# Kernel optimization log

Measured on AMD Instinct MI355X. Metric: run time of the kernel, lower is better.

## Reference

```python
import jax, jax.numpy as jnp
import numpy as np

N = 200000   # active voxels
G = 128      # dense grid extent per axis
C = 128      # hidden channels
IN_C = 1
TEMB = 6
K = 27       # 3x3x3 kernel offsets


def _build_neighbors():
    # Sample N unique voxel coordinates in a G^3 grid and build the 27-offset
    # rulebook: neighbor_idx[k, i] = index of voxel at coord[i] + offset[k],
    # or N (sentinel -> zero-padded feature row) if inactive.
    rng = np.random.default_rng(0)
    lin = np.sort(rng.choice(G ** 3, size=N, replace=False)).astype(np.int64)
    x, r = lin // (G * G), lin % (G * G)
    y, z = r // G, r % G
    nidx = np.full((K, N), N, dtype=np.int32)
    k = 0
    for dx in (-1, 0, 1):
        for dy in (-1, 0, 1):
            for dz in (-1, 0, 1):
                nx, ny, nz = x + dx, y + dy, z + dz
                valid = (nx >= 0) & (nx < G) & (ny >= 0) & (ny < G) & (nz >= 0) & (nz < G)
                key = nx * (G * G) + ny * G + nz
                pos = np.searchsorted(lin, key)
                posc = np.clip(pos, 0, N - 1)
                found = valid & (lin[posc] == key)
                nidx[k] = np.where(found, posc, N).astype(np.int32)
                k += 1
    return jnp.asarray(nidx)


def setup_inputs() -> dict:
    key = jax.random.key(0)
    ks = jax.random.split(key, 8)
    s = jnp.float32(0.05)
    return {
        "features": jax.random.normal(ks[0], (N, IN_C), jnp.float32),
        "t": jax.random.randint(ks[1], (N,), 0, 1000, jnp.int32),
        "neighbor_idx": _build_neighbors(),
        "W1": jax.random.normal(ks[2], (K, IN_C + TEMB, C), jnp.float32) * s,
        "b1": jnp.zeros((C,), jnp.float32),
        "W2": jax.random.normal(ks[3], (K, C, C), jnp.float32) * s,
        "b2": jnp.zeros((C,), jnp.float32),
        "W3": jax.random.normal(ks[4], (C, C), jnp.float32) * s,
        "b3": jnp.zeros((C,), jnp.float32),
        "W4": jax.random.normal(ks[5], (C, 1), jnp.float32) * s,
        "b4": jnp.zeros((1,), jnp.float32),
    }


def _sinusoidal(t, dim):
    half = dim // 2
    freqs = (2.0 ** jnp.arange(half, dtype=jnp.float32)) * jnp.pi  # 2^k * pi
    ang = t.astype(jnp.float32)[:, None] * freqs[None, :]
    return jnp.concatenate([jnp.sin(ang), jnp.cos(ang)], -1)  # [N, dim]


def _sparse_conv3(x, W, b, nidx):
    # Submanifold sparse 3x3x3 conv: for each of 27 offsets, gather neighbor
    # features (zero row for missing) and accumulate a [Cin,Cout] matmul.
    xpad = jnp.concatenate([x, jnp.zeros((1, x.shape[1]), x.dtype)], 0)  # sentinel row
    acc0 = jnp.zeros((x.shape[0], W.shape[-1]), x.dtype)

    def step(acc, kw):
        idx, Wk = kw
        return acc + xpad[idx] @ Wk, None

    acc, _ = jax.lax.scan(step, acc0, (nidx, W))
    return acc + b


def reference(features, t, neighbor_idx, W1, b1, W2, b2, W3, b3, W4, b4):
    # time-embedding concat  [N, 1+6]
    x = jnp.concatenate([features, _sinusoidal(t, TEMB)], -1)
    # SparseConv3d(k=3) + Dropout(eval: identity) + SiLU
    h = jax.nn.silu(_sparse_conv3(x, W1, b1, neighbor_idx))
    h = jax.nn.silu(_sparse_conv3(h, W2, b2, neighbor_idx))
    # SparseConv3d(k=1) + SiLU  == pointwise matmul
    h = jax.nn.silu(h @ W3 + b3)
    # final 1x1 conv to out_channels=1
    return h @ W4 + b4
```

## Files before the change

kernel.cpp:

```cpp
#include <hip/hip_runtime.h>
#include <math.h>

#define N_VOX 200000
#define CCH   128
#define KOFF  27

typedef __attribute__((ext_vector_type(8))) short bf16x8;
typedef __attribute__((ext_vector_type(4))) float f32x4;

__device__ __forceinline__ float silu_f(float x) {
    return x / (1.0f + expf(-x));
}
__device__ __forceinline__ unsigned short f2bf(float x) {
    unsigned int u = __float_as_uint(x);
    u = (u + 0x7FFFu + ((u >> 16) & 1u)) >> 16;
    return (unsigned short)u;
}
__device__ __forceinline__ int xcd_swz(int orig, int nwg) {
    int q = nwg >> 3, r = nwg & 7;
    int xcd = orig & 7, pos = orig >> 3;
    return (xcd < r ? xcd * (q + 1) : r * (q + 1) + (xcd - r) * q) + pos;
}
__device__ __forceinline__ void gload_lds16(const void* g, void* l) {
    __builtin_amdgcn_global_load_lds(
        (const __attribute__((address_space(1))) unsigned int*)g,
        (__attribute__((address_space(3))) unsigned int*)l, 16, 0, 0);
}

__global__ void embed_kernel(const float* __restrict__ feat,
                             const int* __restrict__ t,
                             unsigned short* __restrict__ xeb) {
    int i = blockIdx.x * blockDim.x + threadIdx.x;
    if (i > N_VOX) return;
    union { unsigned short u[8]; int4 v; } o;
    if (i == N_VOX) {
        o.v = make_int4(0, 0, 0, 0);
    } else {
        o.u[0] = f2bf(feat[i]);
        float tf = (float)t[i];
#pragma unroll
        for (int kk = 0; kk < 3; ++kk) {
            float freq = (float)M_PI * (float)(1 << kk);
            float ang = tf * freq;
            o.u[1 + kk] = f2bf(sinf(ang));
            o.u[4 + kk] = f2bf(cosf(ang));
        }
        o.u[7] = 0;
    }
    *(int4*)(xeb + (size_t)i * 8) = o.v;
}

__global__ void convert_w1(const float* __restrict__ W1,
                           unsigned short* __restrict__ W1f) {
    int g = blockIdx.x * 256 + threadIdx.x;
    if (g >= 7 * 8 * 64) return;
    int l = g & 63;
    int rest = g >> 6;
    int nf = rest & 7;
    int kk = rest >> 3;
    int o = kk * 4 + (l >> 4);
    int co = nf * 16 + (l & 15);
    union { unsigned short u[8]; int4 v; } out;
#pragma unroll
    for (int j = 0; j < 8; ++j) {
        float w = 0.f;
        if (o < KOFF && j < 7) w = W1[((size_t)o * 7 + j) * CCH + co];
        out.u[j] = f2bf(w);
    }
    *(int4*)(W1f + (size_t)g * 8) = out.v;
}

__global__ void convert_w2(const float* __restrict__ W2,
                           unsigned short* __restrict__ W2f) {
    int g = blockIdx.x * 256 + threadIdx.x;
    int l = g & 63;
    int rest = g >> 6;
    int nf = rest & 7;
    int kkk = rest >> 3;
    int k = kkk >> 2, kk = kkk & 3;
    int ci0 = kk * 32 + (l >> 4) * 8;
    int co = nf * 16 + (l & 15);
    union { unsigned short u[8]; int4 v; } out;
#pragma unroll
    for (int j = 0; j < 8; ++j)
        out.u[j] = f2bf(W2[((size_t)k * CCH + ci0 + j) * CCH + co]);
    *(int4*)(W2f + (size_t)g * 8) = out.v;
}

__global__ void convert_w3(const float* __restrict__ W3,
                           unsigned short* __restrict__ W3f) {
    int g = blockIdx.x * 256 + threadIdx.x;
    if (g >= 4 * 8 * 64) return;
    int l = g & 63;
    int rest = g >> 6;
    int nf = rest & 7;
    int kk = rest >> 3;
    int ci0 = kk * 32 + (l >> 4) * 8;
    int co = nf * 16 + (l & 15);
    union { unsigned short u[8]; int4 v; } out;
#pragma unroll
    for (int j = 0; j < 8; ++j)
        out.u[j] = f2bf(W3[(size_t)(ci0 + j) * CCH + co]);
    *(int4*)(W3f + (size_t)g * 8) = out.v;
}

__global__ __launch_bounds__(256) void conv1_mfma(
    const unsigned short* __restrict__ xeb, const int* __restrict__ nidx,
    const unsigned short* __restrict__ W1f, const float* __restrict__ b1,
    unsigned short* __restrict__ h1b) {
    __shared__ int4 bufmem[2048];
    __shared__ int idxAll[128 * 28];

    int tid = threadIdx.x;
    int l = tid & 63, w = tid >> 6;
    int mw = w >> 1, nwv = w & 1;
    int wg = xcd_swz(blockIdx.x, gridDim.x);
    int v0 = wg * 128;

    for (int g = tid; g < KOFF * 128; g += 256) {
        int k = g >> 7, vi = g & 127;
        int v = v0 + vi;
        idxAll[vi * 28 + k] = (v < N_VOX) ? nidx[(size_t)k * N_VOX + v] : N_VOX;
    }
    if (tid < 128) idxAll[tid * 28 + 27] = N_VOX;
    __syncthreads();

    f32x4 acc[4][4];
#pragma unroll
    for (int m = 0; m < 4; ++m)
#pragma unroll
        for (int n = 0; n < 4; ++n) acc[m][n] = (f32x4)0.f;

    {
        int4 g0[2]; int rr[2], cc[2];
#pragma unroll
        for (int u = 0; u < 2; ++u) {
            int q = u * 256 + tid;
            int r = q >> 2, oo = q & 3;
            int idx = idxAll[r * 28 + oo];
            g0[u] = *(const int4*)(xeb + (size_t)idx * 8);
            rr[u] = r; cc[u] = oo ^ (r & 3);
        }
#pragma unroll
        for (int u = 0; u < 2; ++u) bufmem[rr[u] * 5 + cc[u]] = g0[u];
    }
    __syncthreads();

    for (int kk = 0; kk < 7; ++kk) {
        int cur = kk & 1;
        int4 gg[2]; int rr[2], cc[2];
        if (kk < 6) {
#pragma unroll
            for (int u = 0; u < 2; ++u) {
                int q = u * 256 + tid;
                int r = q >> 2, oo = q & 3;
                int idx = idxAll[r * 28 + (kk + 1) * 4 + oo];
                gg[u] = *(const int4*)(xeb + (size_t)idx * 8);
                rr[u] = r; cc[u] = oo ^ (r & 3);
            }
        }
        bf16x8 a[4], b[4];
#pragma unroll
        for (int n = 0; n < 4; ++n) {
            int nf = nwv * 4 + n;
            b[n] = *(const bf16x8*)(W1f + ((size_t)(kk * 8 + nf) * 64 + l) * 8);
        }
#pragma unroll
        for (int m = 0; m < 4; ++m) {
            int r = mw * 64 + m * 16 + (l & 15);
            int c = l >> 4;
            a[m] = *(const bf16x8*)&bufmem[cur * 640 + r * 5 + (c ^ (r & 3))];
        }
#pragma unroll
        for (int m = 0; m < 4; ++m)
#pragma unroll
            for (int n = 0; n < 4; ++n)
                acc[m][n] = __builtin_amdgcn_mfma_f32_16x16x32_bf16(
                    a[m], b[n], acc[m][n], 0, 0, 0);
        if (kk < 6) {
#pragma unroll
            for (int u = 0; u < 2; ++u)
                bufmem[(cur ^ 1) * 640 + rr[u] * 5 + cc[u]] = gg[u];
        }
        __syncthreads();
    }

    float bias[4];
#pragma unroll
    for (int n = 0; n < 4; ++n) bias[n] = b1[nwv * 64 + n * 16 + (l & 15)];
    unsigned short* H16 = (unsigned short*)bufmem;
#pragma unroll
    for (int m = 0; m < 4; ++m) {
        int rbase = mw * 64 + m * 16 + (l >> 4) * 4;
#pragma unroll
        for (int n = 0; n < 4; ++n) {
            int ch = nwv * 64 + n * 16 + (l & 15);
            int c = ch >> 3;
            f32x4 d = acc[m][n];
#pragma unroll
            for (int ri = 0; ri < 4; ++ri) {
                int r = rbase + ri;
                int s = (c & 8) | ((c & 7) ^ (r & 7));
                H16[r * 128 + s * 8 + (ch & 7)] = f2bf(silu_f(d[ri] + bias[n]));
            }
        }
    }
    __syncthreads();
#pragma unroll
    for (int u = 0; u < 8; ++u) {
        int q = u * 256 + tid;
        int r = q >> 4, s = q & 15;
        int c = (s & 8) | ((s & 7) ^ (r & 7));
        int v = v0 + r;
        if (v < N_VOX)
            *(int4*)(h1b + (size_t)v * CCH + c * 8) = bufmem[r * 16 + s];
    }
    if (blockIdx.x == 0 && tid < 16)
        *(int4*)(h1b + (size_t)N_VOX * CCH + tid * 8) = make_int4(0, 0, 0, 0);
}

#define STAGE2(bufsel, kq) {                                               \
    _Pragma("unroll") for (int u = 0; u < 8; ++u) {                        \
        int q = u * 256 + tid;                                             \
        int r = q >> 4, s = q & 15;                                        \
        int c = (s & 8) | ((s & 7) ^ (r & 7));                             \
        int idx = idxAll[(kq) * 128 + r];                                  \
        gload_lds16((const char*)h1b + ((size_t)idx << 8) + (c << 4),      \
                    (void*)&Abuf[bufsel][q]);                              \
    }                                                                      \
}

__global__ __launch_bounds__(256, 2) void conv2_mfma(
    const unsigned short* __restrict__ h1b, const int* __restrict__ nidx,
    const unsigned short* __restrict__ W2f, const float* __restrict__ b2,
    const unsigned short* __restrict__ W3f, const float* __restrict__ b3,
    const float* __restrict__ W4, const float* __restrict__ b4,
    float* __restrict__ out) {
    __shared__ int4 Abuf[2][2048];
    __shared__ int idxAll[KOFF * 128];

    int tid = threadIdx.x;
    int l = tid & 63, w = tid >> 6;
    int mw = w >> 1, nwv = w & 1;
    int wg = xcd_swz(blockIdx.x, gridDim.x);
    int v0 = wg * 128;

    for (int g = tid; g < KOFF * 128; g += 256) {
        int k = g >> 7, vi = g & 127;
        int v = v0 + vi;
        idxAll[k * 128 + vi] = (v < N_VOX) ? nidx[(size_t)k * N_VOX + v] : N_VOX;
    }
    __syncthreads();

    f32x4 acc[4][4];
#pragma unroll
    for (int m = 0; m < 4; ++m)
#pragma unroll
        for (int n = 0; n < 4; ++n) acc[m][n] = (f32x4)0.f;

    STAGE2(0, 0);
    asm volatile("s_waitcnt vmcnt(0)" ::: "memory");
    __builtin_amdgcn_s_barrier();

    for (int k = 0; k < KOFF; ++k) {
        int cur = k & 1;
        const unsigned short* wb = W2f + (size_t)k * 16384;
        bf16x8 bf[4][4];
#pragma unroll
        for (int kk = 0; kk < 4; ++kk)
#pragma unroll
            for (int n = 0; n < 4; ++n)
                bf[kk][n] = *(const bf16x8*)(wb +
                    ((size_t)(kk * 8 + nwv * 4 + n) * 64 + l) * 8);
        __builtin_amdgcn_sched_barrier(0);
        if (k + 1 < KOFF) { STAGE2(cur ^ 1, k + 1); }
        __builtin_amdgcn_sched_barrier(0);
#pragma unroll
        for (int kk = 0; kk < 4; ++kk) {
            bf16x8 a[4];
#pragma unroll
            for (int m = 0; m < 4; ++m) {
                int r = mw * 64 + m * 16 + (l & 15);
                int c = kk * 4 + (l >> 4);
                int s = (c & 8) | ((c & 7) ^ (r & 7));
                a[m] = *(const bf16x8*)&Abuf[cur][r * 16 + s];
            }
#pragma unroll
            for (int m = 0; m < 4; ++m)
#pragma unroll
                for (int n = 0; n < 4; ++n)
                    acc[m][n] = __builtin_amdgcn_mfma_f32_16x16x32_bf16(
                        a[m], bf[kk][n], acc[m][n], 0, 0, 0);
        }
        asm volatile("s_waitcnt vmcnt(0)" ::: "memory");
        __builtin_amdgcn_s_barrier();
    }

    float bias2[4];
#pragma unroll
    for (int n = 0; n < 4; ++n) bias2[n] = b2[nwv * 64 + n * 16 + (l & 15)];
    unsigned short* H16 = (unsigned short*)&Abuf[0][0];
#pragma unroll
    for (int m = 0; m < 4; ++m) {
        int rbase = mw * 64 + m * 16 + (l >> 4) * 4;
#pragma unroll
        for (int n = 0; n < 4; ++n) {
            int ch = nwv * 64 + n * 16 + (l & 15);
            int c = ch >> 3;
            f32x4 d = acc[m][n];
#pragma unroll
            for (int ri = 0; ri < 4; ++ri) {
                int r = rbase + ri;
                int s = (c & 8) | ((c & 7) ^ (r & 7));
                H16[r * 128 + s * 8 + (ch & 7)] = f2bf(silu_f(d[ri] + bias2[n]));
            }
        }
    }
    __syncthreads();

    f32x4 p[4][4];
#pragma unroll
    for (int m = 0; m < 4; ++m)
#pragma unroll
        for (int n = 0; n < 4; ++n) p[m][n] = (f32x4)0.f;
#pragma unroll
    for (int kk = 0; kk < 4; ++kk) {
        bf16x8 a[4], b[4];
#pragma unroll
        for (int n = 0; n < 4; ++n) {
            int nf = nwv * 4 + n;
            b[n] = *(const bf16x8*)(W3f + ((size_t)(kk * 8 + nf) * 64 + l) * 8);
        }
#pragma unroll
        for (int m = 0; m < 4; ++m) {
            int r = mw * 64 + m * 16 + (l & 15);
            int c = kk * 4 + (l >> 4);
            int s = (c & 8) | ((c & 7) ^ (r & 7));
            a[m] = *(const bf16x8*)&H16[r * 128 + s * 8];
        }
#pragma unroll
        for (int m = 0; m < 4; ++m)
#pragma unroll
            for (int n = 0; n < 4; ++n)
                p[m][n] = __builtin_amdgcn_mfma_f32_16x16x32_bf16(
                    a[m], b[n], p[m][n], 0, 0, 0);
    }

    float w4v[4], b3v[4];
#pragma unroll
    for (int n = 0; n < 4; ++n) {
        int ch = nwv * 64 + n * 16 + (l & 15);
        w4v[n] = W4[ch];
        b3v[n] = b3[ch];
    }
    float* Osum = (float*)idxAll;
#pragma unroll
    for (int m = 0; m < 4; ++m) {
        float po[4] = {0.f, 0.f, 0.f, 0.f};
#pragma unroll
        for (int n = 0; n < 4; ++n) {
            f32x4 d = p[m][n];
#pragma unroll
            for (int ri = 0; ri < 4; ++ri)
                po[ri] += silu_f(d[ri] + b3v[n]) * w4v[n];
        }
#pragma unroll
        for (int off = 1; off < 16; off <<= 1)
#pragma unroll
            for (int ri = 0; ri < 4; ++ri)
                po[ri] += __shfl_xor(po[ri], off, 64);
        if ((l & 15) == 0) {
            int rbase = mw * 64 + m * 16 + (l >> 4) * 4;
#pragma unroll
            for (int ri = 0; ri < 4; ++ri)
                Osum[nwv * 128 + rbase + ri] = po[ri];
        }
    }
    __syncthreads();
    if (tid < 128) {
        int v = v0 + tid;
        if (v < N_VOX) out[v] = Osum[tid] + Osum[128 + tid] + b4[0];
    }
}

extern "C" void kernel_launch(void* const* d_in, const int* in_sizes, int n_in,
                              void* d_out, int out_size, void* d_ws,
                              size_t ws_size, hipStream_t stream) {
    const float* feat = (const float*)d_in[0];
    const int* t      = (const int*)d_in[1];
    const int* nidx   = (const int*)d_in[2];
    const float* W1   = (const float*)d_in[3];
    const float* b1   = (const float*)d_in[4];
    const float* W2   = (const float*)d_in[5];
    const float* b2   = (const float*)d_in[6];
    const float* W3   = (const float*)d_in[7];
    const float* b3   = (const float*)d_in[8];
    const float* W4   = (const float*)d_in[9];
    const float* b4   = (const float*)d_in[10];
    float* out = (float*)d_out;

    char* ws = (char*)d_ws;
    size_t off = 0;
    unsigned short* xeb = (unsigned short*)(ws + off);
    off += ((size_t)(N_VOX + 1) * 8 * 2 + 255) & ~(size_t)255;
    unsigned short* h1b = (unsigned short*)(ws + off);
    off += ((size_t)(N_VOX + 1) * CCH * 2 + 255) & ~(size_t)255;
    unsigned short* W1f = (unsigned short*)(ws + off);
    off += ((size_t)7 * 8 * 64 * 8 * 2 + 255) & ~(size_t)255;
    unsigned short* W2f = (unsigned short*)(ws + off);
    off += ((size_t)KOFF * 4 * 8 * 64 * 8 * 2 + 255) & ~(size_t)255;
    unsigned short* W3f = (unsigned short*)(ws + off);

    int grid1 = (N_VOX + 127) / 128;
    int grid2 = (N_VOX + 127) / 128;
    embed_kernel<<<(N_VOX + 1 + 255) / 256, 256, 0, stream>>>(feat, t, xeb);
    convert_w1<<<(7 * 8 * 64 + 255) / 256, 256, 0, stream>>>(W1, W1f);
    convert_w2<<<(KOFF * 4 * 8 * 64) / 256, 256, 0, stream>>>(W2, W2f);
    convert_w3<<<(4 * 8 * 64 + 255) / 256, 256, 0, stream>>>(W3, W3f);
    conv1_mfma<<<grid1, 256, 0, stream>>>(xeb, nidx, W1f, b1, h1b);
    conv2_mfma<<<grid2, 256, 0, stream>>>(h1b, nidx, W2f, b2, W3f, b3, W4, b4, out);
}
```

Measured before the change: 296.5 us.

## Compact active neighbors per offset in conv2 and scatter partial products

conv2 no longer gathers all 128 rows for every offset. For each non-center offset it ballot-compacts only the voxels whose neighbor exists (at most 64 per tile) and runs MFMAs on 32-row chunks of that list. The partial products are staged in LDS and scatter-added back into the accumulators, with the scatter for one chunk overlapping the loads for the next. The center offset is still computed densely straight from global memory, and the launch bound is raised to 3 blocks per CU. The intent is to skip the wasted gathers and MFMAs on sentinel rows. The cost is extra syncs and popcount scatter logic, plus silent truncation if an offset ever has more than 64 active neighbors in a tile.

Result: slower. 304.9 us (+2.8%).

```diff
diff --git a/kernel.cpp b/kernel.cpp
--- a/kernel.cpp
+++ b/kernel.cpp
@@ -219,25 +219,52 @@
         *(int4*)(h1b + (size_t)N_VOX * CCH + tid * 8) = make_int4(0, 0, 0, 0);
 }
 
-#define STAGE2(bufsel, kq) {                                               \
-    _Pragma("unroll") for (int u = 0; u < 8; ++u) {                        \
-        int q = u * 256 + tid;                                             \
-        int r = q >> 4, s = q & 15;                                        \
-        int c = (s & 8) | ((s & 7) ^ (r & 7));                             \
-        int idx = idxAll[(kq) * 128 + r];                                  \
-        gload_lds16((const char*)h1b + ((size_t)idx << 8) + (c << 4),      \
-                    (void*)&Abuf[bufsel][q]);                              \
+#define SMEM_P     8192
+#define SMEM_BK    32768
+#define PSTRIDE    36
+
+#define SCATTER(KK, C2) {                                                  \
+    const float* _Pf = (const float*)(smem + SMEM_P);                      \
+    unsigned _w0 = maskL[(KK) * 4 + 2 * mw];                               \
+    unsigned _w1 = maskL[(KK) * 4 + 2 * mw + 1];                           \
+    unsigned _b0 = baseL[(KK) * 4 + 2 * mw];                               \
+    unsigned _b1 = baseL[(KK) * 4 + 2 * mw + 1];                           \
+    int _lo4 = (l >> 4) * 4;                                               \
+    _Pragma("unroll")                                                      \
+    for (int _m = 0; _m < 4; ++_m) {                                       \
+        unsigned _wd = (_m < 2) ? _w0 : _w1;                               \
+        unsigned _bs = (_m < 2) ? _b0 : _b1;                               \
+        int _sh = (_m & 1) * 16 + _lo4;                                    \
+        _Pragma("unroll")                                                  \
+        for (int _ri = 0; _ri < 4; ++_ri) {                                \
+            if ((_wd >> (_sh + _ri)) & 1u) {                               \
+                int _p = _bs +                                             \
+                    __popc(_wd & ((1u << (_sh + _ri)) - 1u));              \
+                int _pr = _p - (C2) * 32;                                  \
+                if (_pr >= 0 && _pr < 32) {                                \
+                    _Pragma("unroll")                                      \
+                    for (int _n = 0; _n < 4; ++_n) {                       \
+                        int _ch = nwv * 64 + _n * 16 + (l & 15);           \
+                        acc[_m][_n][_ri] += _Pf[_ch * PSTRIDE + _pr];      \
+                    }                                                      \
+                }                                                          \
+            }                                                              \
+        }                                                                  \
     }                                                                      \
 }
 
-__global__ __launch_bounds__(256, 2) void conv2_mfma(
+__global__ __launch_bounds__(256, 3) void conv2_mfma(
     const unsigned short* __restrict__ h1b, const int* __restrict__ nidx,
     const unsigned short* __restrict__ W2f, const float* __restrict__ b2,
     const unsigned short* __restrict__ W3f, const float* __restrict__ b3,
     const float* __restrict__ W4, const float* __restrict__ b4,
     float* __restrict__ out) {
-    __shared__ int4 Abuf[2][2048];
-    __shared__ int idxAll[KOFF * 128];
+    __shared__ char smem[SMEM_BK + 6912 + 432 + 432 + 112];
+
+    int* jlistL      = (int*)(smem + SMEM_BK);
+    unsigned* maskL  = (unsigned*)(smem + SMEM_BK + 6912);
+    unsigned* baseL  = maskL + KOFF * 4;
+    int* cntL        = (int*)(baseL + KOFF * 4);
 
     int tid = threadIdx.x;
     int l = tid & 63, w = tid >> 6;
@@ -245,10 +272,33 @@
     int wg = xcd_swz(blockIdx.x, gridDim.x);
     int v0 = wg * 128;
 
-    for (int g = tid; g < KOFF * 128; g += 256) {
-        int k = g >> 7, vi = g & 127;
-        int v = v0 + vi;
-        idxAll[k * 128 + vi] = (v < N_VOX) ? nidx[(size_t)k * N_VOX + v] : N_VOX;
+    for (int i = tid; i < KOFF * 64; i += 256) jlistL[i] = N_VOX;
+    __syncthreads();
+    for (int k = w; k < KOFF; k += 4) {
+        int v1 = v0 + l, v2 = v0 + 64 + l;
+        int j1 = (v1 < N_VOX) ? nidx[(size_t)k * N_VOX + v1] : N_VOX;
+        int j2 = (v2 < N_VOX) ? nidx[(size_t)k * N_VOX + v2] : N_VOX;
+        bool f1 = (k != 13) && (j1 != N_VOX);
+        bool f2 = (k != 13) && (j2 != N_VOX);
+        unsigned long long bal1 = __ballot(f1);
+        unsigned long long bal2 = __ballot(f2);
+        unsigned long long lt = ((unsigned long long)1 << l) - 1;
+        int p1 = __popcll(bal1 & lt);
+        int p2 = __popcll(bal1) + __popcll(bal2 & lt);
+        if (f1 && p1 < 64) jlistL[k * 64 + p1] = j1;
+        if (f2 && p2 < 64) jlistL[k * 64 + p2] = j2;
+        if (l == 0) {
+            unsigned m0 = (unsigned)bal1, m1 = (unsigned)(bal1 >> 32);
+            unsigned m2 = (unsigned)bal2, m3 = (unsigned)(bal2 >> 32);
+            maskL[k * 4 + 0] = m0; maskL[k * 4 + 1] = m1;
+            maskL[k * 4 + 2] = m2; maskL[k * 4 + 3] = m3;
+            unsigned c0 = __popc(m0), c1 = __popc(m1), c2 = __popc(m2);
+            baseL[k * 4 + 0] = 0;
+            baseL[k * 4 + 1] = c0;
+            baseL[k * 4 + 2] = c0 + c1;
+            baseL[k * 4 + 3] = c0 + c1 + c2;
+            cntL[k] = c0 + c1 + c2 + __popc(m3);
+        }
     }
     __syncthreads();
 
@@ -257,49 +307,98 @@
     for (int m = 0; m < 4; ++m)
 #pragma unroll
         for (int n = 0; n < 4; ++n) acc[m][n] = (f32x4)0.f;
-
-    STAGE2(0, 0);
-    asm volatile("s_waitcnt vmcnt(0)" ::: "memory");
-    __builtin_amdgcn_s_barrier();
-
-    for (int k = 0; k < KOFF; ++k) {
-        int cur = k & 1;
-        const unsigned short* wb = W2f + (size_t)k * 16384;
-        bf16x8 bf[4][4];
-#pragma unroll
-        for (int kk = 0; kk < 4; ++kk)
+    {
+        const unsigned short* wb = W2f + (size_t)13 * 16384;
+#pragma unroll
+        for (int kk = 0; kk < 4; ++kk) {
+            bf16x8 a[4], b[4];
+#pragma unroll
+            for (int m = 0; m < 4; ++m) {
+                int v = v0 + mw * 64 + m * 16 + (l & 15);
+                if (v >= N_VOX) v = N_VOX;
+                a[m] = *(const bf16x8*)(h1b + (size_t)v * CCH +
+                                        kk * 32 + (l >> 4) * 8);
+            }
 #pragma unroll
             for (int n = 0; n < 4; ++n)
-                bf[kk][n] = *(const bf16x8*)(wb +
+                b[n] = *(const bf16x8*)(wb +
                     ((size_t)(kk * 8 + nwv * 4 + n) * 64 + l) * 8);
-        __builtin_amdgcn_sched_barrier(0);
-        if (k + 1 < KOFF) { STAGE2(cur ^ 1, k + 1); }
-        __builtin_amdgcn_sched_barrier(0);
-#pragma unroll
-        for (int kk = 0; kk < 4; ++kk) {
-            bf16x8 a[4];
-#pragma unroll
-            for (int m = 0; m < 4; ++m) {
-                int r = mw * 64 + m * 16 + (l & 15);
-                int c = kk * 4 + (l >> 4);
-                int s = (c & 8) | ((c & 7) ^ (r & 7));
-                a[m] = *(const bf16x8*)&Abuf[cur][r * 16 + s];
-            }
 #pragma unroll
             for (int m = 0; m < 4; ++m)
 #pragma unroll
                 for (int n = 0; n < 4; ++n)
                     acc[m][n] = __builtin_amdgcn_mfma_f32_16x16x32_bf16(
-                        a[m], bf[kk][n], acc[m][n], 0, 0, 0);
-        }
-        asm volatile("s_waitcnt vmcnt(0)" ::: "memory");
-        __builtin_amdgcn_s_barrier();
-    }
+                        a[m], b[n], acc[m][n], 0, 0, 0);
+        }
+    }
+
+    float* Pf = (float*)(smem + SMEM_P);
+    int pk = -1, pc2 = 0;
+    for (int k = 0; k < KOFF; ++k) {
+        int cnt = cntL[k];
+        if (cnt == 0) continue;
+        int nch = (cnt + 31) >> 5;
+        if (nch > 2) nch = 2;
+        for (int c2 = 0; c2 < nch; ++c2) {
+#pragma unroll
+            for (int uu = 0; uu < 2; ++uu) {
+                int R = w * 2 + uu, mc = R >> 2, ks = R & 3;
+                int slot = c2 * 32 + mc * 16 + (l & 15);
+                int j = jlistL[k * 64 + slot];
+                gload_lds16((const char*)h1b + (size_t)j * 256 +
+                                ks * 64 + (l >> 4) * 16,
+                            smem + (size_t)(R * 64 + l) * 16);
+            }
+            bf16x8 bfr[4][2];
+            {
+                const unsigned short* wb = W2f + (size_t)k * 16384;
+#pragma unroll
+                for (int ks = 0; ks < 4; ++ks)
+#pragma unroll
+                    for (int nc = 0; nc < 2; ++nc)
+                        bfr[ks][nc] = *(const bf16x8*)(wb +
+                            ((size_t)(ks * 8 + w * 2 + nc) * 64 + l) * 8);
+            }
+            if (pk >= 0) { SCATTER(pk, pc2); }
+            __syncthreads();
+            f32x4 accc[2][2];
+#pragma unroll
+            for (int mc = 0; mc < 2; ++mc)
+#pragma unroll
+                for (int nc = 0; nc < 2; ++nc) accc[mc][nc] = (f32x4)0.f;
+#pragma unroll
+            for (int ks = 0; ks < 4; ++ks) {
+                bf16x8 a2[2];
+#pragma unroll
+                for (int mc = 0; mc < 2; ++mc)
+                    a2[mc] = *(const bf16x8*)(smem +
+                        (size_t)((mc * 4 + ks) * 64 + l) * 16);
+#pragma unroll
+                for (int mc = 0; mc < 2; ++mc)
+#pragma unroll
+                    for (int nc = 0; nc < 2; ++nc)
+                        accc[mc][nc] = __builtin_amdgcn_mfma_f32_16x16x32_bf16(
+                            a2[mc], bfr[ks][nc], accc[mc][nc], 0, 0, 0);
+            }
+#pragma unroll
+            for (int mc = 0; mc < 2; ++mc)
+#pragma unroll
+                for (int nc = 0; nc < 2; ++nc) {
+                    int col = w * 32 + nc * 16 + (l & 15);
+                    int prow = mc * 16 + (l >> 4) * 4;
+                    *(f32x4*)&Pf[col * PSTRIDE + prow] = accc[mc][nc];
+                }
+            __syncthreads();
+            pk = k; pc2 = c2;
+        }
+    }
+    if (pk >= 0) { SCATTER(pk, pc2); }
+    __syncthreads();
 
     float bias2[4];
 #pragma unroll
     for (int n = 0; n < 4; ++n) bias2[n] = b2[nwv * 64 + n * 16 + (l & 15)];
-    unsigned short* H16 = (unsigned short*)&Abuf[0][0];
+    unsigned short* H16 = (unsigned short*)smem;
 #pragma unroll
     for (int m = 0; m < 4; ++m) {
         int rbase = mw * 64 + m * 16 + (l >> 4) * 4;
@@ -353,7 +452,7 @@
         w4v[n] = W4[ch];
         b3v[n] = b3[ch];
     }
-    float* Osum = (float*)idxAll;
+    float* Osum = (float*)jlistL;
 #pragma unroll
     for (int m = 0; m < 4; ++m) {
         float po[4] = {0.f, 0.f, 0.f, 0.f};
@@ -408,7 +507,7 @@
     unsigned short* W1f = (unsigned short*)(ws + off);
     off += ((size_t)7 * 8 * 64 * 8 * 2 + 255) & ~(size_t)255;
     unsigned short* W2f = (unsigned short*)(ws + off);
-    off += ((size_t)KOFF * 4 * 8 * 64 * 8 * 2 + 255) & ~(size_t)255;
+    off += ((size_t)(KOFF + 1) * 4 * 8 * 64 * 8 * 2 + 255) & ~(size_t)255;
     unsigned short* W3f = (unsigned short*)(ws + off);
 
     int grid1 = (N_VOX + 127) / 128;
```
